# Kernel tuning notes

Measured on AMD Instinct MI355X. Metric: run time of the kernel, lower is better.

## Reference

```python
import jax, jax.numpy as jnp
import numpy as np

BS, L, D, CACHE = 8, 2048, 2048, 64   # sequences, tokens/seq, embed_dim, cache rows
T = BS * L
EPS = 1e-6


def setup_inputs() -> dict:
    key = jax.random.key(0)
    ks = jax.random.split(key, 7)
    inputs = jax.random.normal(ks[0], (T, D), jnp.float32)
    lf1_caches = jax.random.normal(ks[1], (CACHE, D), jnp.float32)
    lf2_caches = jax.random.normal(ks[2], (CACHE, D // 2), jnp.float32)
    conv1_weight = jax.random.normal(ks[3], (D, D), jnp.float32) * 0.02
    conv2_weight = jax.random.normal(ks[4], (D // 2, 2 * D), jnp.float32) * 0.02
    conv1_bias = jax.random.normal(ks[5], (D // 2,), jnp.float32) * 0.02
    conv2_bias = jax.random.normal(ks[6], (D,), jnp.float32) * 0.02
    ln_weight = jnp.ones((D,), jnp.float32)
    # consistent continuous-batching layout: each sequence s occupies rows
    # [s*(L+1) .. s*(L+1)+L] of the padded buffer: [cache_tok, tok0..tok_{L-1}]
    s = np.arange(BS, dtype=np.int64)
    j = np.arange(L, dtype=np.int64)
    pre_lf_indexs = jnp.asarray(s)                                  # cache slot per seq
    out_lf_indexs = jnp.asarray(s)
    input_lf_loc = jnp.asarray(s * (L + 1))                         # where cache row goes
    out_lf_loc = jnp.asarray(s * (L + 1) + L)                       # last token -> cache
    inputs_loc = jnp.asarray((s[:, None] * (L + 1) + 1 + j[None, :]).reshape(-1))
    outputs_loc = jnp.asarray((s[:, None] * (L + 1) + j[None, :]).reshape(-1))
    return {
        "inputs": inputs, "pre_lf_indexs": pre_lf_indexs, "out_lf_indexs": out_lf_indexs,
        "input_lf_loc": input_lf_loc, "out_lf_loc": out_lf_loc,
        "inputs_loc": inputs_loc, "outputs_loc": outputs_loc,
        "lf1_caches": lf1_caches, "lf2_caches": lf2_caches,
        "conv1_weight": conv1_weight, "conv2_weight": conv2_weight,
        "conv1_bias": conv1_bias, "conv2_bias": conv2_bias, "ln_weight": ln_weight,
    }


def _fused_cat_conv2d(x, cache, pre_idx, in_lf_loc, in_loc, out_loc, W):
    # scatter tokens + gathered cache rows into padded buffer [T+bs, d]
    bs = pre_idx.shape[0]
    xt = jnp.zeros((x.shape[0] + bs, x.shape[1]), x.dtype)
    xt = xt.at[in_loc].set(x).at[in_lf_loc].set(cache[pre_idx])
    c = xt @ W                                  # [T+bs, 2h]
    h = c.shape[1] // 2
    y = c[:-1, :h] + c[1:, h:]                  # kernel-2 causal conv via shift-add
    return y[out_loc]                           # [T, h]


def reference(inputs, pre_lf_indexs, out_lf_indexs, input_lf_loc, out_lf_loc,
              inputs_loc, outputs_loc, lf1_caches, lf2_caches,
              conv1_weight, conv2_weight, conv1_bias, conv2_bias, ln_weight):
    o1 = _fused_cat_conv2d(inputs, lf1_caches, pre_lf_indexs, input_lf_loc,
                           inputs_loc, outputs_loc, conv1_weight) + conv1_bias
    o2 = _fused_cat_conv2d(o1, lf2_caches, pre_lf_indexs, input_lf_loc,
                           inputs_loc, outputs_loc, conv2_weight) + conv2_bias
    o3 = o2 + inputs
    var = jnp.mean(o3 * o3, axis=-1, keepdims=True)          # RMSNorm
    return o3 * jax.lax.rsqrt(var + EPS) * ln_weight
```

## Files before the change

### kernel.cpp

```cpp
#include <hip/hip_runtime.h>
#include <hip/hip_bf16.h>
#include <stdint.h>

#define T_TOK   16384
#define BSQ     8
#define D1      2048
#define D2      1024

typedef __attribute__((ext_vector_type(8))) short bf16x8;
typedef __attribute__((ext_vector_type(4))) float f32x4;

__device__ __forceinline__ void gll16(const void* g, void* l) {
  __builtin_amdgcn_global_load_lds(
      (const __attribute__((address_space(1))) void*)g,
      (__attribute__((address_space(3))) void*)l, 16, 0, 0);
}

__global__ __launch_bounds__(256) void transpose_all(
    const float* __restrict__ W1, const float* __restrict__ W2,
    __hip_bfloat16* __restrict__ bt1, __hip_bfloat16* __restrict__ bt2) {
  __shared__ float tile[32][33];
  int job = blockIdx.x >> 11;
  int i = blockIdx.x & 2047;
  const float* in; __hip_bfloat16* out;
  int Cin, ldout, c0, kout0, bx, by;
  if (job < 2) {
    in = W1; out = bt1; Cin = 2048; ldout = 4096;
    c0 = job ? 1024 : 0; kout0 = job ? 2048 : 0;
    bx = (i & 31) * 32; by = (i >> 5) * 32;
  } else {
    in = W2; out = bt2; Cin = 4096; ldout = 2048;
    c0 = (job == 3) ? 2048 : 0; kout0 = (job == 3) ? 1024 : 0;
    bx = (i & 63) * 32; by = (i >> 6) * 32;
  }
  int tx = threadIdx.x, ty = threadIdx.y;
  #pragma unroll
  for (int q = 0; q < 32; q += 8)
    tile[ty + q][tx] = in[(size_t)(by + ty + q) * Cin + c0 + bx + tx];
  __syncthreads();
  #pragma unroll
  for (int q = 0; q < 32; q += 8)
    out[(size_t)(bx + ty + q) * ldout + kout0 + by + tx] =
        __float2bfloat16(tile[tx][ty + q]);
}

__global__ __launch_bounds__(256) void prologue(
    const float* __restrict__ x, const int* __restrict__ loc,
    const float* __restrict__ lf1, const float* __restrict__ lf2,
    const int* __restrict__ pre, const int* __restrict__ lfloc,
    __hip_bfloat16* __restrict__ xt1, __hip_bfloat16* __restrict__ xt2) {
  int b = blockIdx.x;
  if (b < T_TOK) {
    int c = threadIdx.x * 8;
    int r = loc[b];
    const float* src = x + (size_t)b * 2048 + c;
    float4 v0 = *(const float4*)src;
    float4 v1 = *(const float4*)(src + 4);
    union { __hip_bfloat16 h[8]; uint4 u; } o;
    o.h[0] = __float2bfloat16(v0.x); o.h[1] = __float2bfloat16(v0.y);
    o.h[2] = __float2bfloat16(v0.z); o.h[3] = __float2bfloat16(v0.w);
    o.h[4] = __float2bfloat16(v1.x); o.h[5] = __float2bfloat16(v1.y);
    o.h[6] = __float2bfloat16(v1.z); o.h[7] = __float2bfloat16(v1.w);
    *(uint4*)(xt1 + (size_t)r * 2048 + c) = o.u;
  } else if (b < T_TOK + BSQ) {
    int s = b - T_TOK;
    int dst = lfloc[s];
    const float* src = lf1 + (size_t)pre[s] * 2048;
    for (int c = threadIdx.x; c < 2048; c += 256)
      xt1[(size_t)dst * 2048 + c] = __float2bfloat16(src[c]);
  } else {
    int s = b - T_TOK - BSQ;
    int dst = lfloc[s];
    const float* src = lf2 + (size_t)pre[s] * 1024;
    for (int c = threadIdx.x; c < 1024; c += 256)
      xt2[(size_t)dst * 1024 + c] = __float2bfloat16(src[c]);
  }
}

template <int EPI>
__global__ __launch_bounds__(256, 4) void gemm_conv(
    const __hip_bfloat16* __restrict__ A0,
    const __hip_bfloat16* __restrict__ Bt,
    const float* __restrict__ bias,
    const float* __restrict__ resid,
    __hip_bfloat16* __restrict__ outb,
    float* __restrict__ outf,
    int N, int K, int KH, int ldA) {
  __shared__ __align__(16) __hip_bfloat16 sA[128 * 32];
  __shared__ __align__(16) __hip_bfloat16 sB[128 * 32];
  const int tid = threadIdx.x;
  const int wave = tid >> 6, lane = tid & 63;
  const int wm = wave & 1, wn = wave >> 1;
  const int tn = blockIdx.x, tm = blockIdx.y;
  const int s = tm >> 4;
  const size_t r0 = (size_t)tm * 128 + s;

  const __hip_bfloat16* Bb = Bt + (size_t)tn * 128 * K;

  const int srow = wave * 16 + (lane >> 2);
  const int scol = (lane & 3) * 8;

  f32x4 acc[4][4];
  #pragma unroll
  for (int i = 0; i < 4; ++i)
    #pragma unroll
    for (int j = 0; j < 4; ++j)
      #pragma unroll
      for (int e = 0; e < 4; ++e) acc[i][j][e] = 0.0f;

  const int frow = lane & 15;
  const int fk = (lane >> 4) * 8;

  #pragma unroll 1
  for (int seg = 0; seg < 2; ++seg) {
    const __hip_bfloat16* Ar = A0 + (r0 + seg) * ldA;
    const __hip_bfloat16* Bs = Bb + seg * KH;
    #pragma unroll 1
    for (int k0 = 0; k0 < KH; k0 += 32) {
      gll16(Ar + (size_t)srow * ldA + k0 + scol,        sA + (wave * 16) * 32);
      gll16(Ar + (size_t)(64 + srow) * ldA + k0 + scol, sA + (64 + wave * 16) * 32);
      gll16(Bs + (size_t)srow * K + k0 + scol,          sB + (wave * 16) * 32);
      gll16(Bs + (size_t)(64 + srow) * K + k0 + scol,   sB + (64 + wave * 16) * 32);
      __builtin_amdgcn_s_waitcnt(0);
      __syncthreads();

      bf16x8 af[4], bfr[4];
      #pragma unroll
      for (int i = 0; i < 4; ++i)
        af[i] = *(const bf16x8*)(sA + (wm * 64 + i * 16 + frow) * 32 + fk);
      #pragma unroll
      for (int j = 0; j < 4; ++j)
        bfr[j] = *(const bf16x8*)(sB + (wn * 64 + j * 16 + frow) * 32 + fk);
      #pragma unroll
      for (int i = 0; i < 4; ++i)
        #pragma unroll
        for (int j = 0; j < 4; ++j)
          acc[i][j] = __builtin_amdgcn_mfma_f32_16x16x32_bf16(af[i], bfr[j], acc[i][j], 0, 0, 0);
      __syncthreads();
    }
  }

  const int t0 = tm * 128 + wm * 64 + (lane >> 4) * 4;
  const int ccol = tn * 128 + wn * 64 + (lane & 15);
  float bj[4];
  #pragma unroll
  for (int j = 0; j < 4; ++j) bj[j] = bias[ccol + j * 16];

  #pragma unroll
  for (int i = 0; i < 4; ++i)
    #pragma unroll
    for (int p = 0; p < 4; ++p) {
      int t = t0 + i * 16 + p;
      if (EPI == 1) {
        __hip_bfloat16* dst = outb + ((size_t)t + s + 1) * N + ccol;
        #pragma unroll
        for (int j = 0; j < 4; ++j)
          dst[j * 16] = __float2bfloat16(acc[i][j][p] + bj[j]);
      } else {
        const float* rsrc = resid + (size_t)t * N + ccol;
        float* dst = outf + (size_t)t * N + ccol;
        #pragma unroll
        for (int j = 0; j < 4; ++j)
          dst[j * 16] = acc[i][j][p] + bj[j] + rsrc[j * 16];
      }
    }
}

__global__ __launch_bounds__(256) void rmsnorm(
    const float* __restrict__ o3, const float* __restrict__ lnw,
    float* __restrict__ out) {
  __shared__ float red[4];
  int t = blockIdx.x;
  int d = threadIdx.x * 8;
  const float* p = o3 + (size_t)t * 2048 + d;
  float o[8];
  *(float4*)&o[0] = *(const float4*)p;
  *(float4*)&o[4] = *(const float4*)(p + 4);
  float ss = 0.0f;
  #pragma unroll
  for (int k = 0; k < 8; ++k) ss += o[k] * o[k];
  #pragma unroll
  for (int off = 32; off > 0; off >>= 1) ss += __shfl_down(ss, off, 64);
  if ((threadIdx.x & 63) == 0) red[threadIdx.x >> 6] = ss;
  __syncthreads();
  float tot = red[0] + red[1] + red[2] + red[3];
  float sc = rsqrtf(tot * (1.0f / 2048.0f) + 1e-6f);
  float lw[8], res[8];
  *(float4*)&lw[0] = *(const float4*)(lnw + d);
  *(float4*)&lw[4] = *(const float4*)(lnw + d + 4);
  #pragma unroll
  for (int k = 0; k < 8; ++k) res[k] = o[k] * sc * lw[k];
  float* dst = out + (size_t)t * 2048 + d;
  *(float4*)dst = *(float4*)&res[0];
  *(float4*)(dst + 4) = *(float4*)&res[4];
}

extern "C" void kernel_launch(void* const* d_in, const int* in_sizes, int n_in,
                              void* d_out, int out_size, void* d_ws, size_t ws_size,
                              hipStream_t stream) {
  const float* inputs = (const float*)d_in[0];
  const int* pre_idx  = (const int*)d_in[1];
  const int* in_lf_loc = (const int*)d_in[3];
  const int* in_loc  = (const int*)d_in[5];
  const float* lf1 = (const float*)d_in[7];
  const float* lf2 = (const float*)d_in[8];
  const float* W1 = (const float*)d_in[9];
  const float* W2 = (const float*)d_in[10];
  const float* b1 = (const float*)d_in[11];
  const float* b2 = (const float*)d_in[12];
  const float* lnw = (const float*)d_in[13];
  float* out = (float*)d_out;

  char* ws = (char*)d_ws;
  float* o3 = (float*)ws;
  __hip_bfloat16* xt1 = (__hip_bfloat16*)(ws + 134217728ull);
  __hip_bfloat16* xt2 = (__hip_bfloat16*)(ws + 201359360ull);
  __hip_bfloat16* bt1 = (__hip_bfloat16*)(ws + 234930176ull);
  __hip_bfloat16* bt2 = (__hip_bfloat16*)(ws + 243318784ull);

  transpose_all<<<8192, dim3(32, 8), 0, stream>>>(W1, W2, bt1, bt2);
  prologue<<<T_TOK + 2 * BSQ, 256, 0, stream>>>(
      inputs, in_loc, lf1, lf2, pre_idx, in_lf_loc, xt1, xt2);

  gemm_conv<1><<<dim3(8, 128), 256, 0, stream>>>(
      xt1, bt1, b1, nullptr, xt2, nullptr, 1024, 4096, 2048, 2048);

  gemm_conv<2><<<dim3(16, 128), 256, 0, stream>>>(
      xt2, bt2, b2, inputs, nullptr, o3, 2048, 2048, 1024, 1024);

  rmsnorm<<<T_TOK, 256, 0, stream>>>(o3, lnw, out);
}
```

Before: 687.4 us.

## Rewrite conv GEMMs with 256x256 tiles, double-buffered LDS and XOR swizzle

Both conv GEMM kernels are replaced by a 512-thread, 256x256-tile version. It uses K=64 stages, double-buffered LDS (128 KB dynamic) with async global-to-LDS prefetch two stages ahead, an XOR-swizzled LDS layout to avoid bank conflicts, and XCD-aware block remapping. The goal is more data reuse per tile and overlap of loads with MFMA work, replacing the old wait-all-then-compute loop. In exchange, each block uses far more registers and LDS, so occupancy drops and the grids get small (256 and 512 blocks), which risks tail and occupancy effects.

```diff
diff --git a/kernel.cpp b/kernel.cpp
--- a/kernel.cpp
+++ b/kernel.cpp
@@ -78,87 +78,137 @@
 }
 
 template <int EPI>
-__global__ __launch_bounds__(256, 4) void gemm_conv(
+__global__ __launch_bounds__(512, 2) void gemm_conv256(
     const __hip_bfloat16* __restrict__ A0,
     const __hip_bfloat16* __restrict__ Bt,
     const float* __restrict__ bias,
     const float* __restrict__ resid,
     __hip_bfloat16* __restrict__ outb,
     float* __restrict__ outf,
-    int N, int K, int KH, int ldA) {
-  __shared__ __align__(16) __hip_bfloat16 sA[128 * 32];
-  __shared__ __align__(16) __hip_bfloat16 sB[128 * 32];
+    int N, int K, int KH, int ldA, int tnBits) {
+  extern __shared__ char smem[];
   const int tid = threadIdx.x;
   const int wave = tid >> 6, lane = tid & 63;
   const int wm = wave & 1, wn = wave >> 1;
-  const int tn = blockIdx.x, tm = blockIdx.y;
-  const int s = tm >> 4;
-  const size_t r0 = (size_t)tm * 128 + s;
-
-  const __hip_bfloat16* Bb = Bt + (size_t)tn * 128 * K;
-
-  const int srow = wave * 16 + (lane >> 2);
-  const int scol = (lane & 3) * 8;
-
-  f32x4 acc[4][4];
-  #pragma unroll
-  for (int i = 0; i < 4; ++i)
+
+  const int nwg = gridDim.x;
+  const int bid = blockIdx.x;
+  const int lb = (bid & 7) * (nwg >> 3) + (bid >> 3);
+  const int tn = lb & ((1 << tnBits) - 1);
+  const int tm = lb >> tnBits;
+
+  const int s = tm >> 3;
+  const size_t r0 = (size_t)tm * 256 + s;
+  const int NTH = KH >> 6;
+  const int NT = NTH * 2;
+
+  const __hip_bfloat16* Bb = Bt + (size_t)tn * 256 * K;
+
+  const int rloc = tid >> 3;
+  const int c8 = (((tid & 7) ^ (rloc & 7)) << 3);
+
+  const int frow = lane & 15;
+  const int xr = (lane & 7) << 3;
+  const int fk = (lane >> 4) << 3;
+  const int ek0 = fk ^ xr;
+  const int ek1 = (fk | 32) ^ xr;
+  int aoff[8], boff[4];
+  #pragma unroll
+  for (int i = 0; i < 8; ++i) aoff[i] = (wm * 128 + i * 16 + frow) * 64;
+  #pragma unroll
+  for (int j = 0; j < 4; ++j) boff[j] = (wn * 64 + j * 16 + frow) * 64;
+
+  f32x4 acc[8][4];
+  #pragma unroll
+  for (int i = 0; i < 8; ++i)
     #pragma unroll
     for (int j = 0; j < 4; ++j)
       #pragma unroll
       for (int e = 0; e < 4; ++e) acc[i][j][e] = 0.0f;
 
-  const int frow = lane & 15;
-  const int fk = (lane >> 4) * 8;
+  auto stage = [&](int buf, int t) {
+    int seg = (t >= NTH) ? 1 : 0;
+    int kk = (t - (seg ? NTH : 0)) << 6;
+    const __hip_bfloat16* Ar = A0 + (r0 + seg) * (size_t)ldA + kk + c8;
+    const __hip_bfloat16* Bs = Bb + (seg ? KH : 0) + kk + c8;
+    char* sbase = smem + buf * 65536 + wave * 1024;
+    #pragma unroll
+    for (int h = 0; h < 2; ++h)
+      #pragma unroll
+      for (int l = 0; l < 2; ++l) {
+        int grow = h * 128 + l * 64 + rloc;
+        gll16(Ar + (size_t)grow * ldA, sbase + h * 16384 + l * 8192);
+        gll16(Bs + (size_t)grow * K,   sbase + 32768 + h * 16384 + l * 8192);
+      }
+  };
+
+  stage(0, 0);
+  stage(1, 1);
+  asm volatile("s_waitcnt vmcnt(8)" ::: "memory");
+  __builtin_amdgcn_s_barrier();
+  asm volatile("" ::: "memory");
 
   #pragma unroll 1
-  for (int seg = 0; seg < 2; ++seg) {
-    const __hip_bfloat16* Ar = A0 + (r0 + seg) * ldA;
-    const __hip_bfloat16* Bs = Bb + seg * KH;
-    #pragma unroll 1
-    for (int k0 = 0; k0 < KH; k0 += 32) {
-      gll16(Ar + (size_t)srow * ldA + k0 + scol,        sA + (wave * 16) * 32);
-      gll16(Ar + (size_t)(64 + srow) * ldA + k0 + scol, sA + (64 + wave * 16) * 32);
-      gll16(Bs + (size_t)srow * K + k0 + scol,          sB + (wave * 16) * 32);
-      gll16(Bs + (size_t)(64 + srow) * K + k0 + scol,   sB + (64 + wave * 16) * 32);
-      __builtin_amdgcn_s_waitcnt(0);
-      __syncthreads();
-
-      bf16x8 af[4], bfr[4];
+  for (int t = 0; t < NT; t += 2) {
+    #pragma unroll
+    for (int half = 0; half < 2; ++half) {
+      const int tt = t + half;
+      const __hip_bfloat16* sT = (const __hip_bfloat16*)(smem + half * 65536);
+      const __hip_bfloat16* sB = sT + 16384;
+
+      __builtin_amdgcn_s_setprio(1);
       #pragma unroll
-      for (int i = 0; i < 4; ++i)
-        af[i] = *(const bf16x8*)(sA + (wm * 64 + i * 16 + frow) * 32 + fk);
-      #pragma unroll
-      for (int j = 0; j < 4; ++j)
-        bfr[j] = *(const bf16x8*)(sB + (wn * 64 + j * 16 + frow) * 32 + fk);
-      #pragma unroll
-      for (int i = 0; i < 4; ++i)
-        #pragma unroll
-        for (int j = 0; j < 4; ++j)
-          acc[i][j] = __builtin_amdgcn_mfma_f32_16x16x32_bf16(af[i], bfr[j], acc[i][j], 0, 0, 0);
-      __syncthreads();
+      for (int k = 0; k < 2; ++k) {
+        const int ek = k ? ek1 : ek0;
+        bf16x8 b[4], a[8];
+        #pragma unroll
+        for (int j = 0; j < 4; ++j) b[j] = *(const bf16x8*)(sB + boff[j] + ek);
+        #pragma unroll
+        for (int i = 0; i < 8; ++i) a[i] = *(const bf16x8*)(sT + aoff[i] + ek);
+        #pragma unroll
+        for (int i = 0; i < 8; ++i)
+          #pragma unroll
+          for (int j = 0; j < 4; ++j)
+            acc[i][j] = __builtin_amdgcn_mfma_f32_16x16x32_bf16(
+                a[i], b[j], acc[i][j], 0, 0, 0);
+      }
+      __builtin_amdgcn_s_setprio(0);
+
+      asm volatile("s_waitcnt lgkmcnt(0)" ::: "memory");
+      __builtin_amdgcn_s_barrier();
+      asm volatile("" ::: "memory");
+
+      if (tt + 2 < NT) {
+        stage(half, tt + 2);
+        __builtin_amdgcn_sched_barrier(0);
+        asm volatile("s_waitcnt vmcnt(8)" ::: "memory");
+      } else {
+        asm volatile("s_waitcnt vmcnt(0)" ::: "memory");
+      }
+      __builtin_amdgcn_s_barrier();
+      asm volatile("" ::: "memory");
     }
   }
 
-  const int t0 = tm * 128 + wm * 64 + (lane >> 4) * 4;
-  const int ccol = tn * 128 + wn * 64 + (lane & 15);
+  const int t0 = tm * 256 + wm * 128 + ((lane >> 4) << 2);
+  const int ccol = tn * 256 + wn * 64 + (lane & 15);
   float bj[4];
   #pragma unroll
   for (int j = 0; j < 4; ++j) bj[j] = bias[ccol + j * 16];
 
   #pragma unroll
-  for (int i = 0; i < 4; ++i)
+  for (int i = 0; i < 8; ++i)
     #pragma unroll
     for (int p = 0; p < 4; ++p) {
-      int t = t0 + i * 16 + p;
+      int tk = t0 + i * 16 + p;
       if (EPI == 1) {
-        __hip_bfloat16* dst = outb + ((size_t)t + s + 1) * N + ccol;
+        __hip_bfloat16* dst = outb + ((size_t)tk + s + 1) * N + ccol;
         #pragma unroll
         for (int j = 0; j < 4; ++j)
           dst[j * 16] = __float2bfloat16(acc[i][j][p] + bj[j]);
       } else {
-        const float* rsrc = resid + (size_t)t * N + ccol;
-        float* dst = outf + (size_t)t * N + ccol;
+        const float* rsrc = resid + (size_t)tk * N + ccol;
+        float* dst = outf + (size_t)tk * N + ccol;
         #pragma unroll
         for (int j = 0; j < 4; ++j)
           dst[j * 16] = acc[i][j][p] + bj[j] + rsrc[j * 16];
@@ -218,15 +268,24 @@
   __hip_bfloat16* bt1 = (__hip_bfloat16*)(ws + 234930176ull);
   __hip_bfloat16* bt2 = (__hip_bfloat16*)(ws + 243318784ull);
 
+  static int lds_inited = 0;
+  if (!lds_inited) {
+    lds_inited = 1;
+    (void)hipFuncSetAttribute(reinterpret_cast<const void*>(&gemm_conv256<1>),
+                              hipFuncAttributeMaxDynamicSharedMemorySize, 131072);
+    (void)hipFuncSetAttribute(reinterpret_cast<const void*>(&gemm_conv256<2>),
+                              hipFuncAttributeMaxDynamicSharedMemorySize, 131072);
+  }
+
   transpose_all<<<8192, dim3(32, 8), 0, stream>>>(W1, W2, bt1, bt2);
   prologue<<<T_TOK + 2 * BSQ, 256, 0, stream>>>(
       inputs, in_loc, lf1, lf2, pre_idx, in_lf_loc, xt1, xt2);
 
-  gemm_conv<1><<<dim3(8, 128), 256, 0, stream>>>(
-      xt1, bt1, b1, nullptr, xt2, nullptr, 1024, 4096, 2048, 2048);
-
-  gemm_conv<2><<<dim3(16, 128), 256, 0, stream>>>(
-      xt2, bt2, b2, inputs, nullptr, o3, 2048, 2048, 1024, 1024);
+  gemm_conv256<1><<<256, 512, 131072, stream>>>(
+      xt1, bt1, b1, nullptr, xt2, nullptr, 1024, 4096, 2048, 2048, 2);
+
+  gemm_conv256<2><<<512, 512, 131072, stream>>>(
+      xt2, bt2, b2, inputs, nullptr, o3, 2048, 2048, 1024, 1024, 3);
 
   rmsnorm<<<T_TOK, 256, 0, stream>>>(o3, lnw, out);
 }
```

Result: faster. 575.8 us (-16.2%).
